# Kernel optimization log

Measured on AMD Instinct MI355X. Metric: run time of the kernel, lower is better.

Reference implementation:

```python
import jax, jax.numpy as jnp
import numpy as np

DIM = 768
H = 12
HD = DIM // H  # 64
TTT_BASE_LR = 1.0
EPS = 1e-6


def ln_fwd(x, gamma, beta):
    mu = jnp.mean(x, axis=-1, keepdims=True)
    var = jnp.mean((x - mu) ** 2, axis=-1, keepdims=True)
    x_hat = (x - mu) / jnp.sqrt(var + EPS)
    return gamma * x_hat + beta


def ln_fused_l2_bwd(x, l2_target, gamma, beta):
    # grad of 0.5*||LN(x)*gamma+beta - target||^2 wrt x
    D = x.shape[-1]
    mu = jnp.mean(x, axis=-1, keepdims=True)
    var = jnp.mean((x - mu) ** 2, axis=-1, keepdims=True)
    std = jnp.sqrt(var + EPS)
    x_hat = (x - mu) / std
    y = gamma * x_hat + beta
    grad_out = y - l2_target
    g = grad_out * gamma
    z = (D * g - jnp.sum(g, -1, keepdims=True)
         - x_hat * jnp.sum(g * x_hat, -1, keepdims=True)) / (D * std)
    return z


def setup_inputs() -> dict:
    key = jax.random.key(0)
    ks = jax.random.split(key, 10)
    B, N, C = 16, 1024, DIM
    return {
        'x': jax.random.normal(ks[0], (B, N, C), jnp.float32),
        'qkv_weight': jax.random.normal(ks[1], (3 * C, C), jnp.float32) * 0.02,
        'q_bias': jnp.zeros((C,), jnp.float32),
        'v_bias': jnp.zeros((C,), jnp.float32),
        'proj_weight': jax.random.normal(ks[2], (C, C), jnp.float32) * 0.02,
        'proj_bias': jnp.zeros((C,), jnp.float32),
        'ttt_lr_weight': jax.random.normal(ks[3], (H, 1, C), jnp.float32) * 0.02,
        'ttt_lr_bias': jnp.zeros((H, 1), jnp.float32),
        'ttt_norm_weight': jnp.ones((H, HD), jnp.float32),
        'ttt_norm_bias': jnp.zeros((H, HD), jnp.float32),
        'W1': jax.random.normal(ks[4], (H, HD, HD), jnp.float32) * 0.02,
        'b1': jnp.zeros((H, 1, HD), jnp.float32),
    }


def reference(x, qkv_weight, q_bias, v_bias, proj_weight, proj_bias,
              ttt_lr_weight, ttt_lr_bias, ttt_norm_weight, ttt_norm_bias,
              W1, b1):
    B, N, C = x.shape
    num_mini_batch = 1  # hardcoded in module
    m = N // num_mini_batch

    # fused qkv (k bias is a zero buffer)
    qkv_bias = jnp.concatenate([q_bias, jnp.zeros_like(q_bias), v_bias])
    qkv = x @ qkv_weight.T + qkv_bias                      # [B,N,3C]
    qkv = qkv.reshape(B, N, 3, H, HD).transpose(2, 0, 3, 1, 4)
    q, k, v = qkv[0], qkv[1], qkv[2]                       # [B,H,N,HD]

    # per-token learnable lr: sigmoid(x @ w_h + b_h), then / head_dim
    ttt_lr = jnp.einsum('bnc,hdc->bhnd', x, ttt_lr_weight) \
             + ttt_lr_bias.reshape(1, H, 1, 1)
    ttt_lr_eta = TTT_BASE_LR * jax.nn.sigmoid(ttt_lr) / HD  # [B,H,N,1]

    gamma = ttt_norm_weight.reshape(H, 1, HD)
    beta = ttt_norm_bias.reshape(H, 1, HD)

    def compute_mini_batch(carry, inp):
        W1c, b1c = carry                                   # [B,H,HD,HD],[B,H,1,HD]
        XQ, XK, XV, eta = inp                              # [B,H,m,HD], eta [B,H,m,1]
        Z1 = XK @ W1c + b1c
        g = ln_fused_l2_bwd(Z1, XV - XK, gamma, beta)
        g = g * eta / m
        grad_W1 = jnp.einsum('bhmd,bhme->bhde', XK, g)
        grad_b1 = jnp.sum(g, axis=2, keepdims=True)
        W1n = W1c - grad_W1
        b1n = b1c - grad_b1
        Z1_bar = ln_fwd(XQ @ W1n + b1n, gamma, beta)
        return (W1n, b1n), XQ + Z1_bar

    def to_scan(t):  # [B,H,N,D] -> [M,B,H,m,D]
        return t.reshape(B, H, num_mini_batch, m, t.shape[-1]).transpose(2, 0, 1, 3, 4)

    xs = (to_scan(q), to_scan(k), to_scan(v), to_scan(ttt_lr_eta))
    init = (jnp.broadcast_to(W1, (B, H, HD, HD)),
            jnp.broadcast_to(b1, (B, H, 1, HD)))
    _, XQW = jax.lax.scan(compute_mini_batch, init, xs)    # [M,B,H,m,HD]
    out = XQW.transpose(1, 2, 0, 3, 4).reshape(B, H, N, HD)

    out = out.transpose(0, 2, 1, 3).reshape(B, N, C)       # [B,N,C]
    out = out @ proj_weight.T + proj_bias
    return out
```

## Files before the change

kernel.cpp:

```cpp
#include <hip/hip_runtime.h>
#include <hip/hip_bf16.h>
#include <math.h>


#define Bdim 16
#define Ndim 1024
#define Cdim 768
#define Hdim 12
#define HDdim 64
#define NCH 8
#define CH 128

typedef __hip_bfloat16 bf16;
typedef short short8 __attribute__((ext_vector_type(8)));
typedef short short4v __attribute__((ext_vector_type(4)));
typedef float f32x4 __attribute__((ext_vector_type(4)));

__device__ __forceinline__ float wred(float v) {
    #pragma unroll
    for (int o = 32; o > 0; o >>= 1) v += __shfl_xor(v, o);
    return v;
}

__device__ __forceinline__ unsigned short f2bf(float f) {
    __hip_bfloat16 h = __float2bfloat16(f);
    return *reinterpret_cast<unsigned short*>(&h);
}

__device__ __forceinline__ void gload_lds16(const bf16* g, bf16* l) {
    __builtin_amdgcn_global_load_lds(
        (const __attribute__((address_space(1))) void*)g,
        (__attribute__((address_space(3))) void*)l, 16, 0, 0);
}

__global__ __launch_bounds__(256) void cast_kernel(
    const float* __restrict__ in, unsigned short* __restrict__ out)
{
    int i = blockIdx.x * 256 + threadIdx.x;
    float4 v = ((const float4*)in)[i];
    short4v o;
    o.x = f2bf(v.x); o.y = f2bf(v.y); o.z = f2bf(v.z); o.w = f2bf(v.w);
    ((short4v*)out)[i] = o;
}

template<int BIAS_MODE>
__global__ __launch_bounds__(256) void gemm_bt_mfma(
    const bf16* __restrict__ A, const bf16* __restrict__ B,
    const float* __restrict__ b0, const float* __restrict__ b1v,
    float* __restrict__ C, int M, int N, int K)
{
    __shared__ bf16 As[128 * 32];
    __shared__ bf16 Bs[128 * 32];
    const int tid = threadIdx.x;
    const int wid = tid >> 6, lane = tid & 63;
    const int row0 = blockIdx.x * 128, col0 = blockIdx.y * 128;

    const int srow = lane >> 2;
    const int scol = (lane & 3) * 8;
    const bf16* Ag[2]; const bf16* Bg[2];
    bf16* Al[2]; bf16* Bl[2];
    #pragma unroll
    for (int j = 0; j < 2; ++j) {
        int chunk = wid * 2 + j;
        int r = chunk * 16 + srow;
        Ag[j] = A + (size_t)(row0 + r) * K + scol;
        Bg[j] = B + (size_t)(col0 + r) * K + scol;
        Al[j] = &As[chunk * 16 * 32];
        Bl[j] = &Bs[chunk * 16 * 32];
    }

    const int wm = (wid >> 1) * 64, wn = (wid & 1) * 64;
    const int fr = lane & 15;
    const int fq = lane >> 4;
    f32x4 acc[4][4] = {};

    for (int k0 = 0; k0 < K; k0 += 32) {
        __syncthreads();
        #pragma unroll
        for (int j = 0; j < 2; ++j) {
            gload_lds16(Ag[j] + k0, Al[j]);
            gload_lds16(Bg[j] + k0, Bl[j]);
        }
        __syncthreads();
        short8 af[4], bfr[4];
        #pragma unroll
        for (int i = 0; i < 4; ++i) {
            af[i]  = *(const short8*)&As[(wm + i * 16 + fr) * 32 + fq * 8];
            bfr[i] = *(const short8*)&Bs[(wn + i * 16 + fr) * 32 + fq * 8];
        }
        #pragma unroll
        for (int mi = 0; mi < 4; ++mi)
            #pragma unroll
            for (int ni = 0; ni < 4; ++ni)
                acc[mi][ni] = __builtin_amdgcn_mfma_f32_16x16x32_bf16(
                    af[mi], bfr[ni], acc[mi][ni], 0, 0, 0);
    }

    #pragma unroll
    for (int ni = 0; ni < 4; ++ni) {
        int ccol = col0 + wn + ni * 16 + fr;
        float bias;
        if (BIAS_MODE == 0) bias = (ccol < 768) ? b0[ccol] : (ccol < 1536 ? 0.f : b1v[ccol - 1536]);
        else                bias = b0[ccol];
        #pragma unroll
        for (int mi = 0; mi < 4; ++mi) {
            #pragma unroll
            for (int r = 0; r < 4; ++r) {
                int crow = row0 + wm + mi * 16 + fq * 4 + r;
                C[(size_t)crow * N + ccol] = acc[mi][ni][r] + bias;
            }
        }
    }
}

__global__ __launch_bounds__(256) void eta_kernel(
    const float* __restrict__ x, const float* __restrict__ lrw,
    const float* __restrict__ lrb, float* __restrict__ eta)
{
    __shared__ float xs[768];
    const int bn = blockIdx.x;
    const int tid = threadIdx.x, lane = tid & 63, w = tid >> 6;
    const float* xrow = x + (size_t)bn * Cdim;
    if (tid < 192) *(float4*)&xs[tid*4] = *(const float4*)&xrow[tid*4];
    __syncthreads();
    const int b = bn >> 10, n = bn & 1023;
    for (int h = w; h < Hdim; h += 4) {
        float p = 0.f;
        const float* wr = lrw + h * Cdim;
        #pragma unroll
        for (int j = 0; j < 12; ++j) p += xs[lane + j*64] * wr[lane + j*64];
        p = wred(p);
        if (lane == 0) {
            float v = p + lrb[h];
            eta[((size_t)b*Hdim + h)*Ndim + n] = (1.f / (1.f + expf(-v))) * 0.015625f;
        }
    }
}

__global__ __launch_bounds__(256) void ttt_init(
    const float* __restrict__ W1g, const float* __restrict__ b1g,
    float* __restrict__ W1n, float* __restrict__ bn1)
{
    const int bh = blockIdx.x, h = bh % Hdim, tid = threadIdx.x;
    #pragma unroll
    for (int j = 0; j < 16; ++j)
        W1n[(size_t)bh * 4096 + j * 256 + tid] = W1g[h * 4096 + j * 256 + tid];
    if (tid < 64) bn1[bh * 64 + tid] = b1g[h * 64 + tid];
}

__global__ __launch_bounds__(256) void ttt_grad(
    const float* __restrict__ qkv,
    const float* __restrict__ eta,
    const float* __restrict__ W1g,
    const float* __restrict__ b1g,
    const float* __restrict__ gammag, const float* __restrict__ betag,
    float* __restrict__ W1n,
    float* __restrict__ bn1)
{
    const int bh = blockIdx.x;
    const int b = bh / Hdim, h = bh % Hdim;
    const int c0base = blockIdx.y * CH;
    const int tid = threadIdx.x, lane = tid & 63, w = tid >> 6;
    const int e = lane, dbase = w * 16;

    __shared__ float W1s[64][64];
    __shared__ float XSs[64][64];
    __shared__ float Gs[64][64];
    __shared__ float b1s[64], gms[64], bts[64];
    __shared__ float gb1p[4][64];

    for (int i = tid; i < 4096; i += 256) ((float*)W1s)[i] = W1g[h*4096 + i];
    if (tid < 64) {
        b1s[tid] = b1g[h*64 + tid];
        gms[tid] = gammag[h*64 + tid];
        bts[tid] = betag[h*64 + tid];
    }
    float acc[16];
    #pragma unroll
    for (int i = 0; i < 16; ++i) acc[i] = 0.f;
    float gb1 = 0.f;

    const float* qkv_b = qkv + (size_t)b * Ndim * 2304 + h * 64;
    const float* eta_b = eta + ((size_t)b * Hdim + h) * Ndim;
    __syncthreads();

    for (int half = 0; half < CH / 64; ++half) {
        const int c0 = c0base + half * 64;
        #pragma unroll
        for (int j = 0; j < 4; ++j) {
            int f = tid + j * 256;
            int r = f >> 4, c4 = (f & 15) << 2;
            *(float4*)&XSs[r][c4] = *(const float4*)(qkv_b + (size_t)(c0 + r)*2304 + 768 + c4);
        }
        __syncthreads();
        #pragma unroll 1
        for (int i = 0; i < 16; ++i) {
            int r = w * 16 + i;
            int n = c0 + r;
            float xk = XSs[r][lane];
            float z = b1s[lane];
            #pragma unroll
            for (int k2 = 0; k2 < 64; ++k2) z += XSs[r][k2] * W1s[k2][lane];
            float mu = wred(z) * 0.015625f;
            float zc = z - mu;
            float var = wred(zc * zc) * 0.015625f;
            float rstd = rsqrtf(var + 1e-6f);
            float xh = zc * rstd;
            float gm = gms[lane];
            float xv = qkv_b[(size_t)n * 2304 + 1536 + lane];
            float etav = eta_b[n];
            float gg = (gm * xh + bts[lane] - (xv - xk)) * gm;
            float s1 = wred(gg);
            float s2 = wred(gg * xh);
            float gf = (64.f * gg - s1 - xh * s2) * rstd * 0.015625f * etav * 0.0009765625f;
            Gs[r][lane] = gf;
            gb1 += gf;
        }
        __syncthreads();
        #pragma unroll 4
        for (int mm = 0; mm < 64; ++mm) {
            float gv = Gs[mm][e];
            #pragma unroll
            for (int i2 = 0; i2 < 16; ++i2) acc[i2] += XSs[mm][dbase + i2] * gv;
        }
        __syncthreads();
    }

    #pragma unroll
    for (int i2 = 0; i2 < 16; ++i2)
        atomicAdd(&W1n[(size_t)bh * 4096 + (dbase + i2) * 64 + e], -acc[i2]);
    gb1p[w][lane] = gb1;
    __syncthreads();
    if (tid < 64) {
        float s = gb1p[0][tid] + gb1p[1][tid] + gb1p[2][tid] + gb1p[3][tid];
        atomicAdd(&bn1[bh * 64 + tid], -s);
    }
}

__global__ __launch_bounds__(256) void ttt_apply(
    const float* __restrict__ qkv,
    const float* __restrict__ W1n, const float* __restrict__ bn1,
    const float* __restrict__ gammag, const float* __restrict__ betag,
    unsigned short* __restrict__ inner)
{
    const int bh = blockIdx.x;
    const int b = bh / Hdim, h = bh % Hdim;
    const int c0base = blockIdx.y * CH;
    const int tid = threadIdx.x, lane = tid & 63, w = tid >> 6;

    __shared__ float W1s[64][64];
    __shared__ float XSs[64][64];
    __shared__ float bn1s[64], gms[64], bts[64];

    for (int i = tid; i < 4096; i += 256) ((float*)W1s)[i] = W1n[(size_t)bh*4096 + i];
    if (tid < 64) {
        bn1s[tid] = bn1[bh*64 + tid];
        gms[tid] = gammag[h*64 + tid];
        bts[tid] = betag[h*64 + tid];
    }
    const float* qkv_b = qkv + (size_t)b * Ndim * 2304 + h * 64;
    __syncthreads();

    for (int half = 0; half < CH / 64; ++half) {
        const int c0 = c0base + half * 64;
        #pragma unroll
        for (int j = 0; j < 4; ++j) {
            int f = tid + j * 256;
            int r = f >> 4, c4 = (f & 15) << 2;
            *(float4*)&XSs[r][c4] = *(const float4*)(qkv_b + (size_t)(c0 + r)*2304 + 0 + c4);
        }
        __syncthreads();
        #pragma unroll 1
        for (int i = 0; i < 16; ++i) {
            int r = w * 16 + i;
            int n = c0 + r;
            float xq = XSs[r][lane];
            float z = bn1s[lane];
            #pragma unroll
            for (int k2 = 0; k2 < 64; ++k2) z += XSs[r][k2] * W1s[k2][lane];
            float mu = wred(z) * 0.015625f;
            float zc = z - mu;
            float var = wred(zc * zc) * 0.015625f;
            float rstd = rsqrtf(var + 1e-6f);
            float xh = zc * rstd;
            inner[(size_t)(b * Ndim + n) * Cdim + h * 64 + lane] =
                f2bf(xq + gms[lane] * xh + bts[lane]);
        }
        __syncthreads();
    }
}

extern "C" void kernel_launch(void* const* d_in, const int* in_sizes, int n_in,
                              void* d_out, int out_size, void* d_ws, size_t ws_size,
                              hipStream_t stream) {
    const float* x     = (const float*)d_in[0];
    const float* qkvw  = (const float*)d_in[1];
    const float* qb    = (const float*)d_in[2];
    const float* vb    = (const float*)d_in[3];
    const float* pw    = (const float*)d_in[4];
    const float* pb    = (const float*)d_in[5];
    const float* lrw   = (const float*)d_in[6];
    const float* lrb   = (const float*)d_in[7];
    const float* gamma = (const float*)d_in[8];
    const float* beta  = (const float*)d_in[9];
    const float* W1    = (const float*)d_in[10];
    const float* b1    = (const float*)d_in[11];
    float* out = (float*)d_out;

    float* qkv = (float*)d_ws;
    float* eta = qkv + (size_t)16384 * 2304;
    unsigned short* inner = (unsigned short*)(eta + 196608);
    unsigned short* xb    = inner + (size_t)16384 * 768;
    unsigned short* qkvwb = xb + (size_t)16384 * 768;
    unsigned short* pwb   = qkvwb + (size_t)2304 * 768;
    float* W1n = (float*)(pwb + (size_t)768 * 768);
    float* bn1 = W1n + (size_t)192 * 4096;

    cast_kernel<<<16384 * 768 / 1024, 256, 0, stream>>>(x, xb);
    cast_kernel<<<2304 * 768 / 1024, 256, 0, stream>>>(qkvw, qkvwb);
    cast_kernel<<<768 * 768 / 1024, 256, 0, stream>>>(pw, pwb);

    gemm_bt_mfma<0><<<dim3(16384 / 128, 2304 / 128), 256, 0, stream>>>(
        (const bf16*)xb, (const bf16*)qkvwb, qb, vb, qkv, 16384, 2304, Cdim);

    eta_kernel<<<Bdim * Ndim, 256, 0, stream>>>(x, lrw, lrb, eta);

    ttt_init<<<Bdim * Hdim, 256, 0, stream>>>(W1, b1, W1n, bn1);
    ttt_grad<<<dim3(Bdim * Hdim, NCH), 256, 0, stream>>>(
        qkv, eta, W1, b1, gamma, beta, W1n, bn1);
    ttt_apply<<<dim3(Bdim * Hdim, NCH), 256, 0, stream>>>(
        qkv, W1n, bn1, gamma, beta, inner);

    gemm_bt_mfma<1><<<dim3(16384 / 128, 768 / 128), 256, 0, stream>>>(
        (const bf16*)inner, (const bf16*)pwb, pb, nullptr, out, 16384, Cdim, Cdim);
}
```

Baseline: 479.6 us.

## Use bf16 MFMA for TTT inner matmuls in grad and apply kernels

Replaces the scalar FP32 64x64 matmuls in ttt_grad (XK@W1 and XK^T@G) and ttt_apply (XQ@W1n) with bf16 MFMA 16x16x32 instructions. Operands are stored in padded bf16 shared-memory tiles, with transposed copies of W1 and XK. Per-row XK, XV and eta values are prefetched into registers before the LayerNorm/gradient pass. This removes the FP32 FMA cost of the inner products but rounds Z1, G and W1 to bf16, which adds precision error to the normalized outputs and the weight update.

```diff
diff --git a/kernel.cpp b/kernel.cpp
--- a/kernel.cpp
+++ b/kernel.cpp
@@ -10,6 +10,7 @@
 #define HDdim 64
 #define NCH 8
 #define CH 128
+#define LSTR 72
 
 typedef __hip_bfloat16 bf16;
 typedef short short8 __attribute__((ext_vector_type(8)));
@@ -25,6 +26,11 @@
 __device__ __forceinline__ unsigned short f2bf(float f) {
     __hip_bfloat16 h = __float2bfloat16(f);
     return *reinterpret_cast<unsigned short*>(&h);
+}
+
+__device__ __forceinline__ float bf2f(unsigned short u) {
+    unsigned int x = ((unsigned int)u) << 16;
+    return __uint_as_float(x);
 }
 
 __device__ __forceinline__ void gload_lds16(const bf16* g, bf16* l) {
@@ -161,74 +167,118 @@
     const int b = bh / Hdim, h = bh % Hdim;
     const int c0base = blockIdx.y * CH;
     const int tid = threadIdx.x, lane = tid & 63, w = tid >> 6;
-    const int e = lane, dbase = w * 16;
-
-    __shared__ float W1s[64][64];
-    __shared__ float XSs[64][64];
-    __shared__ float Gs[64][64];
+    const int fr = lane & 15, fq = lane >> 4;
+
+    __shared__ __align__(16) unsigned short XKs [64 * LSTR];
+    __shared__ __align__(16) unsigned short XKTs[64 * LSTR];
+    __shared__ __align__(16) unsigned short W1Ts[64 * LSTR];
+    __shared__ __align__(16) unsigned short Gst [64 * LSTR];
+    __shared__ __align__(16) unsigned short Z1s [64 * LSTR];
     __shared__ float b1s[64], gms[64], bts[64];
     __shared__ float gb1p[4][64];
 
-    for (int i = tid; i < 4096; i += 256) ((float*)W1s)[i] = W1g[h*4096 + i];
+    for (int i = tid; i < 4096; i += 256) {
+        int d = i >> 6, e = i & 63;
+        W1Ts[e * LSTR + d] = f2bf(W1g[h * 4096 + i]);
+    }
     if (tid < 64) {
         b1s[tid] = b1g[h*64 + tid];
         gms[tid] = gammag[h*64 + tid];
         bts[tid] = betag[h*64 + tid];
     }
-    float acc[16];
-    #pragma unroll
-    for (int i = 0; i < 16; ++i) acc[i] = 0.f;
+    f32x4 gacc[4] = {};
     float gb1 = 0.f;
 
     const float* qkv_b = qkv + (size_t)b * Ndim * 2304 + h * 64;
     const float* eta_b = eta + ((size_t)b * Hdim + h) * Ndim;
     __syncthreads();
 
-    for (int half = 0; half < CH / 64; ++half) {
+    #pragma unroll 1
+    for (int half = 0; half < 2; ++half) {
         const int c0 = c0base + half * 64;
         #pragma unroll
         for (int j = 0; j < 4; ++j) {
             int f = tid + j * 256;
             int r = f >> 4, c4 = (f & 15) << 2;
-            *(float4*)&XSs[r][c4] = *(const float4*)(qkv_b + (size_t)(c0 + r)*2304 + 768 + c4);
-        }
-        __syncthreads();
-        #pragma unroll 1
+            float4 v = *(const float4*)(qkv_b + (size_t)(c0 + r)*2304 + 768 + c4);
+            unsigned short u0 = f2bf(v.x), u1 = f2bf(v.y), u2 = f2bf(v.z), u3 = f2bf(v.w);
+            short4v sv; sv.x = (short)u0; sv.y = (short)u1; sv.z = (short)u2; sv.w = (short)u3;
+            *(short4v*)&XKs[r * LSTR + c4] = sv;
+            XKTs[(c4+0) * LSTR + r] = u0;
+            XKTs[(c4+1) * LSTR + r] = u1;
+            XKTs[(c4+2) * LSTR + r] = u2;
+            XKTs[(c4+3) * LSTR + r] = u3;
+        }
+        __syncthreads();
+        {
+            short8 a0 = *(const short8*)&W1Ts[(w*16 + fr) * LSTR + 0];
+            short8 a1 = *(const short8*)&W1Ts[(w*16 + fr) * LSTR + 32 + fq*8 - fq*8 + fq*8];
+            a1 = *(const short8*)&W1Ts[(w*16 + fr) * LSTR + 32 + fq*8];
+            a0 = *(const short8*)&W1Ts[(w*16 + fr) * LSTR + 0  + fq*8];
+            f32x4 zacc[4] = {};
+            #pragma unroll
+            for (int nt = 0; nt < 4; ++nt) {
+                short8 b0 = *(const short8*)&XKs[(nt*16 + fr) * LSTR + 0  + fq*8];
+                short8 b1_ = *(const short8*)&XKs[(nt*16 + fr) * LSTR + 32 + fq*8];
+                zacc[nt] = __builtin_amdgcn_mfma_f32_16x16x32_bf16(a0, b0, zacc[nt], 0, 0, 0);
+                zacc[nt] = __builtin_amdgcn_mfma_f32_16x16x32_bf16(a1, b1_, zacc[nt], 0, 0, 0);
+            }
+            #pragma unroll
+            for (int nt = 0; nt < 4; ++nt)
+                #pragma unroll
+                for (int rr = 0; rr < 4; ++rr)
+                    Z1s[(nt*16 + fr) * LSTR + (w*16 + fq*4 + rr)] = f2bf(zacc[nt][rr]);
+        }
+        __syncthreads();
+        float xkr[16], xvr[16], etr[16];
+        #pragma unroll
         for (int i = 0; i < 16; ++i) {
-            int r = w * 16 + i;
-            int n = c0 + r;
-            float xk = XSs[r][lane];
-            float z = b1s[lane];
-            #pragma unroll
-            for (int k2 = 0; k2 < 64; ++k2) z += XSs[r][k2] * W1s[k2][lane];
+            int n = c0 + w*16 + i;
+            xkr[i] = qkv_b[(size_t)n * 2304 + 768 + lane];
+            xvr[i] = qkv_b[(size_t)n * 2304 + 1536 + lane];
+            etr[i] = eta_b[n];
+        }
+        #pragma unroll
+        for (int i = 0; i < 16; ++i) {
+            int r = w*16 + i;
+            float z = bf2f(Z1s[r * LSTR + lane]) + b1s[lane];
             float mu = wred(z) * 0.015625f;
             float zc = z - mu;
             float var = wred(zc * zc) * 0.015625f;
             float rstd = rsqrtf(var + 1e-6f);
             float xh = zc * rstd;
             float gm = gms[lane];
-            float xv = qkv_b[(size_t)n * 2304 + 1536 + lane];
-            float etav = eta_b[n];
-            float gg = (gm * xh + bts[lane] - (xv - xk)) * gm;
+            float gg = (gm * xh + bts[lane] - (xvr[i] - xkr[i])) * gm;
             float s1 = wred(gg);
             float s2 = wred(gg * xh);
-            float gf = (64.f * gg - s1 - xh * s2) * rstd * 0.015625f * etav * 0.0009765625f;
-            Gs[r][lane] = gf;
+            float gf = (64.f * gg - s1 - xh * s2) * rstd * 0.015625f * etr[i] * 0.0009765625f;
             gb1 += gf;
-        }
-        __syncthreads();
-        #pragma unroll 4
-        for (int mm = 0; mm < 64; ++mm) {
-            float gv = Gs[mm][e];
-            #pragma unroll
-            for (int i2 = 0; i2 < 16; ++i2) acc[i2] += XSs[mm][dbase + i2] * gv;
+            Gst[lane * LSTR + r] = f2bf(gf);
+        }
+        __syncthreads();
+        {
+            short8 a0 = *(const short8*)&Gst[(w*16 + fr) * LSTR + 0  + fq*8];
+            short8 a1 = *(const short8*)&Gst[(w*16 + fr) * LSTR + 32 + fq*8];
+            #pragma unroll
+            for (int nt = 0; nt < 4; ++nt) {
+                short8 b0 = *(const short8*)&XKTs[(nt*16 + fr) * LSTR + 0  + fq*8];
+                short8 b1_ = *(const short8*)&XKTs[(nt*16 + fr) * LSTR + 32 + fq*8];
+                gacc[nt] = __builtin_amdgcn_mfma_f32_16x16x32_bf16(a0, b0, gacc[nt], 0, 0, 0);
+                gacc[nt] = __builtin_amdgcn_mfma_f32_16x16x32_bf16(a1, b1_, gacc[nt], 0, 0, 0);
+            }
         }
         __syncthreads();
     }
 
     #pragma unroll
-    for (int i2 = 0; i2 < 16; ++i2)
-        atomicAdd(&W1n[(size_t)bh * 4096 + (dbase + i2) * 64 + e], -acc[i2]);
+    for (int nt = 0; nt < 4; ++nt) {
+        int d = nt*16 + fr;
+        #pragma unroll
+        for (int rr = 0; rr < 4; ++rr) {
+            int e = w*16 + fq*4 + rr;
+            atomicAdd(&W1n[(size_t)bh * 4096 + d * 64 + e], -gacc[nt][rr]);
+        }
+    }
     gb1p[w][lane] = gb1;
     __syncthreads();
     if (tid < 64) {
@@ -247,12 +297,17 @@
     const int b = bh / Hdim, h = bh % Hdim;
     const int c0base = blockIdx.y * CH;
     const int tid = threadIdx.x, lane = tid & 63, w = tid >> 6;
-
-    __shared__ float W1s[64][64];
-    __shared__ float XSs[64][64];
+    const int fr = lane & 15, fq = lane >> 4;
+
+    __shared__ __align__(16) unsigned short XQs  [64 * LSTR];
+    __shared__ __align__(16) unsigned short W1nTs[64 * LSTR];
+    __shared__ __align__(16) unsigned short Z1s  [64 * LSTR];
     __shared__ float bn1s[64], gms[64], bts[64];
 
-    for (int i = tid; i < 4096; i += 256) ((float*)W1s)[i] = W1n[(size_t)bh*4096 + i];
+    for (int i = tid; i < 4096; i += 256) {
+        int d = i >> 6, e = i & 63;
+        W1nTs[e * LSTR + d] = f2bf(W1n[(size_t)bh * 4096 + i]);
+    }
     if (tid < 64) {
         bn1s[tid] = bn1[bh*64 + tid];
         gms[tid] = gammag[h*64 + tid];
@@ -261,30 +316,55 @@
     const float* qkv_b = qkv + (size_t)b * Ndim * 2304 + h * 64;
     __syncthreads();
 
-    for (int half = 0; half < CH / 64; ++half) {
+    #pragma unroll 1
+    for (int half = 0; half < 2; ++half) {
         const int c0 = c0base + half * 64;
         #pragma unroll
         for (int j = 0; j < 4; ++j) {
             int f = tid + j * 256;
             int r = f >> 4, c4 = (f & 15) << 2;
-            *(float4*)&XSs[r][c4] = *(const float4*)(qkv_b + (size_t)(c0 + r)*2304 + 0 + c4);
-        }
-        __syncthreads();
-        #pragma unroll 1
+            float4 v = *(const float4*)(qkv_b + (size_t)(c0 + r)*2304 + 0 + c4);
+            short4v sv; sv.x = (short)f2bf(v.x); sv.y = (short)f2bf(v.y);
+            sv.z = (short)f2bf(v.z); sv.w = (short)f2bf(v.w);
+            *(short4v*)&XQs[r * LSTR + c4] = sv;
+        }
+        __syncthreads();
+        {
+            short8 a0 = *(const short8*)&W1nTs[(w*16 + fr) * LSTR + 0  + fq*8];
+            short8 a1 = *(const short8*)&W1nTs[(w*16 + fr) * LSTR + 32 + fq*8];
+            f32x4 zacc[4] = {};
+            #pragma unroll
+            for (int nt = 0; nt < 4; ++nt) {
+                short8 b0 = *(const short8*)&XQs[(nt*16 + fr) * LSTR + 0  + fq*8];
+                short8 b1_ = *(const short8*)&XQs[(nt*16 + fr) * LSTR + 32 + fq*8];
+                zacc[nt] = __builtin_amdgcn_mfma_f32_16x16x32_bf16(a0, b0, zacc[nt], 0, 0, 0);
+                zacc[nt] = __builtin_amdgcn_mfma_f32_16x16x32_bf16(a1, b1_, zacc[nt], 0, 0, 0);
+            }
+            #pragma unroll
+            for (int nt = 0; nt < 4; ++nt)
+                #pragma unroll
+                for (int rr = 0; rr < 4; ++rr)
+                    Z1s[(nt*16 + fr) * LSTR + (w*16 + fq*4 + rr)] = f2bf(zacc[nt][rr]);
+        }
+        __syncthreads();
+        float xqr[16];
+        #pragma unroll
         for (int i = 0; i < 16; ++i) {
-            int r = w * 16 + i;
+            int n = c0 + w*16 + i;
+            xqr[i] = qkv_b[(size_t)n * 2304 + 0 + lane];
+        }
+        #pragma unroll
+        for (int i = 0; i < 16; ++i) {
+            int r = w*16 + i;
             int n = c0 + r;
-            float xq = XSs[r][lane];
-            float z = bn1s[lane];
-            #pragma unroll
-            for (int k2 = 0; k2 < 64; ++k2) z += XSs[r][k2] * W1s[k2][lane];
+            float z = bf2f(Z1s[r * LSTR + lane]) + bn1s[lane];
             float mu = wred(z) * 0.015625f;
             float zc = z - mu;
             float var = wred(zc * zc) * 0.015625f;
             float rstd = rsqrtf(var + 1e-6f);
             float xh = zc * rstd;
             inner[(size_t)(b * Ndim + n) * Cdim + h * 64 + lane] =
-                f2bf(xq + gms[lane] * xh + bts[lane]);
+                f2bf(xqr[i] + gms[lane] * xh + bts[lane]);
         }
         __syncthreads();
     }
```

New measurement: 425.3 us. -11.3%, faster.
